# Optimization experiments

Measured on AMD Instinct MI355X. Metric: run time of the kernel, lower is better.

## Reference

```python
import jax, jax.numpy as jnp
import numpy as np

B, T, N_EMBD, HEAD = 4, 2048, 1024, 128


def setup_inputs() -> dict:
    key = jax.random.key(0)
    ks = jax.random.split(key, 7)
    s = 1.0 / np.sqrt(N_EMBD)
    return {
        "X": jax.random.normal(ks[0], (B, T, N_EMBD), dtype=jnp.float32),
        "Wk": jax.random.normal(ks[1], (N_EMBD, HEAD), dtype=jnp.float32) * s,
        "bk": jax.random.normal(ks[2], (HEAD,), dtype=jnp.float32) * 0.02,
        "Wq": jax.random.normal(ks[3], (N_EMBD, HEAD), dtype=jnp.float32) * s,
        "bq": jax.random.normal(ks[4], (HEAD,), dtype=jnp.float32) * 0.02,
        "Wv": jax.random.normal(ks[5], (N_EMBD, HEAD), dtype=jnp.float32) * s,
        "bv": jax.random.normal(ks[6], (HEAD,), dtype=jnp.float32) * 0.02,
    }


def reference(X, Wk, bk, Wq, bq, Wv, bv):
    # X: [B, T, C] with C = n_embd
    C = X.shape[-1]
    k = X @ Wk + bk  # [B, T, H]
    q = X @ Wq + bq  # [B, T, H]
    # NOTE: original computes k @ q^T (not q @ k^T) and scales by n_embd**-0.5.
    wei = jnp.einsum("bth,bsh->bts", k, q) * (C ** -0.5)  # [B, T, T]
    # NOTE: original's masked_fill is not in-place and its result is discarded,
    # so NO causal mask is actually applied. Dropout is identity (eval).
    wei = jax.nn.softmax(wei, axis=-1)
    v = X @ Wv + bv  # [B, T, H]
    out = jnp.einsum("bts,bsh->bth", wei, v)  # [B, T, H]
    return out
```

## Files before the change

kernel.cpp:

```cpp
#include <hip/hip_runtime.h>
#include <hip/hip_bf16.h>

#define Bn 4
#define Tn 2048
#define Cn 1024
#define Hn 128
#define Mn (Bn*Tn)
#define SCHUNKS 4
#define SCHUNK  (Tn/SCHUNKS)

typedef _Float16 f16;
typedef __attribute__((ext_vector_type(4))) _Float16 f16x4;
typedef __attribute__((ext_vector_type(8))) _Float16 f16x8;
typedef __attribute__((ext_vector_type(4))) float f32x4;

__global__ __launch_bounds__(256) void prep_w(const float* __restrict__ Wk,
                                              const float* __restrict__ Wq,
                                              const float* __restrict__ Wv,
                                              f16* __restrict__ Wt) {
    __shared__ __align__(16) f16 T[64 * 72];
    const int w = blockIdx.z;
    const float* W = (w == 0) ? Wk : (w == 1) ? Wq : Wv;
    const int c0 = blockIdx.x * 64, h0 = blockIdx.y * 64;
    const int tid = threadIdx.x;

    for (int i = 0; i < 4; i++) {
        int ci = tid + 256 * i;
        int row = ci >> 4, c4 = ci & 15;
        float4 x = *(const float4*)(W + (c0 + row) * Hn + h0 + c4 * 4);
        f16x4 v = { (f16)x.x, (f16)x.y, (f16)x.z, (f16)x.w };
        *(f16x4*)(&T[row * 72 + c4 * 4]) = v;
    }
    __syncthreads();
    for (int i = 0; i < 2; i++) {
        int ci = tid + 256 * i;
        int h = ci >> 3, cc = ci & 7;
        f16x8 v;
        for (int j = 0; j < 8; j++) v[j] = T[(cc * 8 + j) * 72 + h];
        *(f16x8*)(Wt + (w * Hn + h0 + h) * Cn + c0 + cc * 8) = v;
    }
}

__global__ __launch_bounds__(512) void qkv_gemm(const float* __restrict__ X,
                                                const f16* __restrict__ Wt,
                                                const float* __restrict__ bk,
                                                const float* __restrict__ bq,
                                                const float* __restrict__ bv,
                                                f16* __restrict__ pk,
                                                f16* __restrict__ pq,
                                                f16* __restrict__ vT) {
    __shared__ __align__(16) char smem[36864];
    f16* As = (f16*)smem;
    f16* Bs = (f16*)(smem + 9216);

    const int tid  = threadIdx.x;
    const int r0   = blockIdx.x * 64;
    const int ns   = blockIdx.y;
    const int lane = tid & 63, wid = tid >> 6;
    const int quad = lane >> 4, l16 = lane & 15;
    const int wm = wid >> 2, wn = wid & 3;

    f32x4 acc[2][3] = {};

    for (int k0 = 0; k0 < Cn; k0 += 64) {
        for (int i = 0; i < 2; i++) {
            int ci = tid + 512 * i;
            int row = ci >> 4, c4 = ci & 15;
            float4 x = *(const float4*)(X + (r0 + row) * Cn + k0 + c4 * 4);
            f16x4 v = { (f16)x.x, (f16)x.y, (f16)x.z, (f16)x.w };
            *(f16x4*)(&As[row * 72 + c4 * 4]) = v;
        }
        for (int i = 0; i < 3; i++) {
            int ci = tid + 512 * i;
            int row = ci >> 3, cc = ci & 7;
            *(f16x8*)(&Bs[row * 72 + cc * 8]) =
                *(const f16x8*)(Wt + (ns * 192 + row) * Cn + k0 + cc * 8);
        }
        __syncthreads();
        for (int ks = 0; ks < 2; ks++) {
            int kk = ks * 32;
            f16x8 af[2], bf[3];
            for (int mt = 0; mt < 2; mt++)
                af[mt] = *(const f16x8*)(&As[(wm * 32 + mt * 16 + l16) * 72 + kk + quad * 8]);
            for (int nt = 0; nt < 3; nt++)
                bf[nt] = *(const f16x8*)(&Bs[(wn * 48 + nt * 16 + l16) * 72 + kk + quad * 8]);
            for (int mt = 0; mt < 2; mt++)
                for (int nt = 0; nt < 3; nt++)
                    acc[mt][nt] = __builtin_amdgcn_mfma_f32_16x16x32_f16(
                        af[mt], bf[nt], acc[mt][nt], 0, 0, 0);
        }
        __syncthreads();
    }

    f16* E = (f16*)smem;
    for (int nt = 0; nt < 3; nt++) {
        int n0 = ns * 192 + wn * 48 + nt * 16;
        int wsel = n0 >> 7;
        int col = (n0 & 127) + l16;
        const float* bias = (wsel == 0) ? bk : (wsel == 1) ? bq : bv;
        float bval = bias[col];
        float scale = (wsel == 0) ? 0.03125f : 1.0f;
        for (int mt = 0; mt < 2; mt++)
            for (int r = 0; r < 4; r++) {
                int mrow = wm * 32 + mt * 16 + quad * 4 + r;
                E[mrow * 200 + wn * 48 + nt * 16 + l16] =
                    (f16)((acc[mt][nt][r] + bval) * scale);
            }
    }
    __syncthreads();

    if (ns == 0) {
        for (int i = 0; i < 3; i++) {
            int ci = tid + 512 * i;
            int row = ci / 24, c = ci % 24;
            f16x8 v = *(const f16x8*)(&E[row * 200 + c * 8]);
            int gn = c * 8;
            f16* dst = (gn < 128) ? (pk + (r0 + row) * Hn + gn)
                                  : (pq + (r0 + row) * Hn + (gn - 128));
            *(f16x8*)dst = v;
        }
    } else {
        {
            int ci = tid;
            int row = ci >> 3, c = ci & 7;
            f16x8 v = *(const f16x8*)(&E[row * 200 + c * 8]);
            *(f16x8*)(pq + (r0 + row) * Hn + 64 + c * 8) = v;
        }
        int b = r0 >> 11, sg = r0 & 2047;
        for (int i = 0; i < 2; i++) {
            int ci = tid + 512 * i;
            int h = ci >> 3, sc = ci & 7;
            f16x8 v;
            for (int j = 0; j < 8; j++)
                v[j] = E[(sc * 8 + j) * 200 + 64 + h];
            *(f16x8*)(vT + (b * Hn + h) * Tn + sg + sc * 8) = v;
        }
    }
}

__global__ __launch_bounds__(256, 2) void attn_kernel(const f16* __restrict__ pk,
                                                      const f16* __restrict__ pq,
                                                      const f16* __restrict__ vT,
                                                      f16* __restrict__ pO,
                                                      float* __restrict__ pm,
                                                      float* __restrict__ pl) {
    __shared__ __align__(16) char smem[36864];
    f16* Bq = (f16*)smem;
    f16* Vt = (f16*)(smem + 17408);

    const int tid  = threadIdx.x;
    const int tblk = blockIdx.x, c = blockIdx.y, b = blockIdx.z;
    const int t0   = tblk * 128;
    const int lane = tid & 63, wid = tid >> 6;
    const int quad = lane >> 4, l16 = lane & 15;
    const int tw   = t0 + wid * 32;

    const f16* kp = pk + b * Tn * Hn;
    const f16* qp = pq + b * Tn * Hn;
    const f16* vp = vT + b * Hn * Tn;

    f16x8 kfr[2][4];
    for (int tt = 0; tt < 2; tt++)
        for (int ks = 0; ks < 4; ks++)
            kfr[tt][ks] = *(const f16x8*)(kp + (tw + tt * 16 + l16) * Hn + ks * 32 + quad * 8);

    float m_i[2] = { -3e38f, -3e38f }, l_i[2] = { 0.0f, 0.0f };
    f32x4 accO[2][8] = {};

    f16x8 qreg[4], vreg[4];
    {
        const int s0 = c * SCHUNK;
        for (int i = 0; i < 4; i++) {
            int ci = tid + 256 * i;
            qreg[i] = *(const f16x8*)(qp + (s0 + (ci >> 4)) * Hn + (ci & 15) * 8);
            vreg[i] = *(const f16x8*)(vp + (ci >> 3) * Tn + s0 + (ci & 7) * 8);
        }
    }

    for (int si = 0; si < SCHUNK / 64; si++) {
        __syncthreads();
        for (int i = 0; i < 4; i++) {
            int ci = tid + 256 * i;
            *(f16x8*)(&Bq[(ci >> 4) * 136 + (ci & 15) * 8]) = qreg[i];
            *(f16x8*)(&Vt[(ci >> 3) * 72 + (ci & 7) * 8]) = vreg[i];
        }
        __syncthreads();
        if (si + 1 < SCHUNK / 64) {
            const int s1 = c * SCHUNK + (si + 1) * 64;
            for (int i = 0; i < 4; i++) {
                int ci = tid + 256 * i;
                qreg[i] = *(const f16x8*)(qp + (s1 + (ci >> 4)) * Hn + (ci & 15) * 8);
                vreg[i] = *(const f16x8*)(vp + (ci >> 3) * Tn + s1 + (ci & 7) * 8);
            }
        }

        f32x4 accS[2][4] = {};
        for (int ks = 0; ks < 4; ks++) {
            int kk = ks * 32;
            for (int st = 0; st < 4; st++) {
                f16x8 af = *(const f16x8*)(&Bq[(st * 16 + l16) * 136 + kk + quad * 8]);
                accS[0][st] = __builtin_amdgcn_mfma_f32_16x16x32_f16(af, kfr[0][ks], accS[0][st], 0, 0, 0);
                accS[1][st] = __builtin_amdgcn_mfma_f32_16x16x32_f16(af, kfr[1][ks], accS[1][st], 0, 0, 0);
            }
        }

        f16x4 pf[2][4];
        for (int tt = 0; tt < 2; tt++) {
            float mloc = -3e38f;
            for (int st = 0; st < 4; st++)
                for (int r = 0; r < 4; r++) mloc = fmaxf(mloc, accS[tt][st][r]);
            mloc = fmaxf(mloc, __shfl_xor(mloc, 16));
            mloc = fmaxf(mloc, __shfl_xor(mloc, 32));
            float mnew = fmaxf(m_i[tt], mloc);
            float alpha = __expf(m_i[tt] - mnew);
            m_i[tt] = mnew;
            float psum = 0.0f;
            for (int st = 0; st < 4; st++) {
                f32x4 p;
                for (int r = 0; r < 4; r++) {
                    p[r] = __expf(accS[tt][st][r] - mnew);
                    psum += p[r];
                }
                pf[tt][st] = { (f16)p[0], (f16)p[1], (f16)p[2], (f16)p[3] };
            }
            psum += __shfl_xor(psum, 16);
            psum += __shfl_xor(psum, 32);
            l_i[tt] = l_i[tt] * alpha + psum;
            for (int ht = 0; ht < 8; ht++)
                for (int r = 0; r < 4; r++) accO[tt][ht][r] *= alpha;
        }

        for (int st = 0; st < 4; st++) {
            for (int ht = 0; ht < 8; ht++) {
                f16x4 av = *(const f16x4*)(&Vt[(ht * 16 + l16) * 72 + st * 16 + quad * 4]);
                accO[0][ht] = __builtin_amdgcn_mfma_f32_16x16x16f16(av, pf[0][st], accO[0][ht], 0, 0, 0);
                accO[1][ht] = __builtin_amdgcn_mfma_f32_16x16x16f16(av, pf[1][st], accO[1][ht], 0, 0, 0);
            }
        }
    }

    for (int tt = 0; tt < 2; tt++) {
        __syncthreads();
        float* ep = (float*)smem + wid * 2048;
        for (int ht = 0; ht < 8; ht++)
            for (int r = 0; r < 4; r++)
                ep[(ht * 16 + quad * 4 + r) * 16 + l16] = accO[tt][ht][r];
        __syncthreads();
        {
            int t = lane >> 2, hq = lane & 3;
            int tgl = tw + tt * 16 + t;
            f16* dst = pO + ((size_t)(c * Bn + b) * Tn + tgl) * Hn + hq * 32;
            for (int g = 0; g < 4; g++) {
                f16x8 v;
                for (int j = 0; j < 8; j++)
                    v[j] = (f16)ep[(hq * 32 + g * 8 + j) * 16 + t];
                *(f16x8*)(dst + g * 8) = v;
            }
        }
        if (quad == 0) {
            pm[(c * Bn + b) * Tn + tw + tt * 16 + l16] = m_i[tt];
            pl[(c * Bn + b) * Tn + tw + tt * 16 + l16] = l_i[tt];
        }
    }
}

__global__ __launch_bounds__(256) void merge_kernel(const f16* __restrict__ pO,
                                                    const float* __restrict__ pm,
                                                    const float* __restrict__ pl,
                                                    float* __restrict__ out) {
    int gid = blockIdx.x * 256 + threadIdx.x;
    int tg  = gid >> 4;
    int hs  = (gid & 15) * 8;
    float mc[SCHUNKS], lc[SCHUNKS];
    float M = -3e38f;
    for (int cI = 0; cI < SCHUNKS; cI++) {
        mc[cI] = pm[cI * (Bn * Tn) + tg];
        lc[cI] = pl[cI * (Bn * Tn) + tg];
        M = fmaxf(M, mc[cI]);
    }
    float L = 0.0f, wc[SCHUNKS];
    for (int cI = 0; cI < SCHUNKS; cI++) {
        wc[cI] = __expf(mc[cI] - M);
        L += wc[cI] * lc[cI];
    }
    float inv = 1.0f / L;
    float o[8] = {};
    for (int cI = 0; cI < SCHUNKS; cI++) {
        const f16* src = pO + ((size_t)cI * Bn * Tn + tg) * Hn + hs;
        f16x8 v = *(const f16x8*)src;
        float w = wc[cI];
        for (int j = 0; j < 8; j++) o[j] += w * (float)v[j];
    }
    float* dst = out + (size_t)tg * Hn + hs;
    float4 v0 = { o[0] * inv, o[1] * inv, o[2] * inv, o[3] * inv };
    float4 v1 = { o[4] * inv, o[5] * inv, o[6] * inv, o[7] * inv };
    *(float4*)dst = v0;
    *(float4*)(dst + 4) = v1;
}

extern "C" void kernel_launch(void* const* d_in, const int* in_sizes, int n_in,
                              void* d_out, int out_size, void* d_ws, size_t ws_size,
                              hipStream_t stream) {
    const float* X  = (const float*)d_in[0];
    const float* Wk = (const float*)d_in[1];
    const float* bk = (const float*)d_in[2];
    const float* Wq = (const float*)d_in[3];
    const float* bq = (const float*)d_in[4];
    const float* Wv = (const float*)d_in[5];
    const float* bv = (const float*)d_in[6];
    float* out = (float*)d_out;

    char* base = (char*)d_ws;
    f16*   Wt = (f16*)(base);
    f16*   pk = (f16*)(base + 786432);
    f16*   pq = (f16*)(base + 2883584);
    f16*   vT = (f16*)(base + 4980736);
    f16*   pO = (f16*)(base + 7077888);
    float* pm = (float*)(base + 15466496);
    float* pl = (float*)(base + 15597568);

    prep_w<<<dim3(Cn / 64, Hn / 64, 3), 256, 0, stream>>>(Wk, Wq, Wv, Wt);
    qkv_gemm<<<dim3(Mn / 64, 2), 512, 0, stream>>>(X, Wt, bk, bq, bv, pk, pq, vT);
    attn_kernel<<<dim3(Tn / 128, SCHUNKS, Bn), 256, 0, stream>>>(pk, pq, vT, pO, pm, pl);
    merge_kernel<<<dim3(512), 256, 0, stream>>>(pO, pm, pl, out);
}
```

Measured before the change: 126.9 us.

## Register-prefetch next K tile in QKV GEMM and halve block to four waves

The QKV projection GEMM now loads the next 64-wide K slice of X and the weights into registers while MFMAs run on the current shared-memory tile, instead of doing load, sync, compute serially. The block shrinks from 512 to 256 threads, with each wave covering all 64 rows and 48 columns (a 4x3 MFMA tile per wave), which doubles per-wave register reuse of B fragments. The cost is more registers per thread (launch bounds 256,1) and fewer waves per block to hide latency.

After: 129.3 us. Within noise of the previous version (+1.9%).

```diff
diff --git a/kernel.cpp b/kernel.cpp
--- a/kernel.cpp
+++ b/kernel.cpp
@@ -41,14 +41,14 @@
     }
 }
 
-__global__ __launch_bounds__(512) void qkv_gemm(const float* __restrict__ X,
-                                                const f16* __restrict__ Wt,
-                                                const float* __restrict__ bk,
-                                                const float* __restrict__ bq,
-                                                const float* __restrict__ bv,
-                                                f16* __restrict__ pk,
-                                                f16* __restrict__ pq,
-                                                f16* __restrict__ vT) {
+__global__ __launch_bounds__(256, 1) void qkv_gemm(const float* __restrict__ X,
+                                                   const f16* __restrict__ Wt,
+                                                   const float* __restrict__ bk,
+                                                   const float* __restrict__ bq,
+                                                   const float* __restrict__ bv,
+                                                   f16* __restrict__ pk,
+                                                   f16* __restrict__ pq,
+                                                   f16* __restrict__ vT) {
     __shared__ __align__(16) char smem[36864];
     f16* As = (f16*)smem;
     f16* Bs = (f16*)(smem + 9216);
@@ -56,41 +56,60 @@
     const int tid  = threadIdx.x;
     const int r0   = blockIdx.x * 64;
     const int ns   = blockIdx.y;
-    const int lane = tid & 63, wid = tid >> 6;
+    const int lane = tid & 63, wn = tid >> 6;
     const int quad = lane >> 4, l16 = lane & 15;
-    const int wm = wid >> 2, wn = wid & 3;
-
-    f32x4 acc[2][3] = {};
-
-    for (int k0 = 0; k0 < Cn; k0 += 64) {
-        for (int i = 0; i < 2; i++) {
-            int ci = tid + 512 * i;
-            int row = ci >> 4, c4 = ci & 15;
-            float4 x = *(const float4*)(X + (r0 + row) * Cn + k0 + c4 * 4);
+
+    f32x4 acc[4][3] = {};
+
+    float4 xreg[4];
+    f16x8  wreg[6];
+    for (int i = 0; i < 4; i++) {
+        int ci = tid + 256 * i;
+        xreg[i] = *(const float4*)(X + (r0 + (ci >> 4)) * Cn + (ci & 15) * 4);
+    }
+    for (int i = 0; i < 6; i++) {
+        int ci = tid + 256 * i;
+        wreg[i] = *(const f16x8*)(Wt + (ns * 192 + (ci >> 3)) * Cn + (ci & 7) * 8);
+    }
+
+    for (int kit = 0; kit < 16; kit++) {
+        __syncthreads();
+        for (int i = 0; i < 4; i++) {
+            int ci = tid + 256 * i;
+            float4 x = xreg[i];
             f16x4 v = { (f16)x.x, (f16)x.y, (f16)x.z, (f16)x.w };
-            *(f16x4*)(&As[row * 72 + c4 * 4]) = v;
-        }
-        for (int i = 0; i < 3; i++) {
-            int ci = tid + 512 * i;
-            int row = ci >> 3, cc = ci & 7;
-            *(f16x8*)(&Bs[row * 72 + cc * 8]) =
-                *(const f16x8*)(Wt + (ns * 192 + row) * Cn + k0 + cc * 8);
-        }
-        __syncthreads();
+            *(f16x4*)(&As[(ci >> 4) * 72 + (ci & 15) * 4]) = v;
+        }
+        for (int i = 0; i < 6; i++) {
+            int ci = tid + 256 * i;
+            *(f16x8*)(&Bs[(ci >> 3) * 72 + (ci & 7) * 8]) = wreg[i];
+        }
+        __syncthreads();
+        if (kit + 1 < 16) {
+            int k1 = (kit + 1) * 64;
+            for (int i = 0; i < 4; i++) {
+                int ci = tid + 256 * i;
+                xreg[i] = *(const float4*)(X + (r0 + (ci >> 4)) * Cn + k1 + (ci & 15) * 4);
+            }
+            for (int i = 0; i < 6; i++) {
+                int ci = tid + 256 * i;
+                wreg[i] = *(const f16x8*)(Wt + (ns * 192 + (ci >> 3)) * Cn + k1 + (ci & 7) * 8);
+            }
+        }
         for (int ks = 0; ks < 2; ks++) {
             int kk = ks * 32;
-            f16x8 af[2], bf[3];
-            for (int mt = 0; mt < 2; mt++)
-                af[mt] = *(const f16x8*)(&As[(wm * 32 + mt * 16 + l16) * 72 + kk + quad * 8]);
+            f16x8 af[4], bf[3];
+            for (int mt = 0; mt < 4; mt++)
+                af[mt] = *(const f16x8*)(&As[(mt * 16 + l16) * 72 + kk + quad * 8]);
             for (int nt = 0; nt < 3; nt++)
                 bf[nt] = *(const f16x8*)(&Bs[(wn * 48 + nt * 16 + l16) * 72 + kk + quad * 8]);
-            for (int mt = 0; mt < 2; mt++)
+            for (int mt = 0; mt < 4; mt++)
                 for (int nt = 0; nt < 3; nt++)
                     acc[mt][nt] = __builtin_amdgcn_mfma_f32_16x16x32_f16(
                         af[mt], bf[nt], acc[mt][nt], 0, 0, 0);
         }
-        __syncthreads();
-    }
+    }
+    __syncthreads();
 
     f16* E = (f16*)smem;
     for (int nt = 0; nt < 3; nt++) {
@@ -100,9 +119,9 @@
         const float* bias = (wsel == 0) ? bk : (wsel == 1) ? bq : bv;
         float bval = bias[col];
         float scale = (wsel == 0) ? 0.03125f : 1.0f;
-        for (int mt = 0; mt < 2; mt++)
+        for (int mt = 0; mt < 4; mt++)
             for (int r = 0; r < 4; r++) {
-                int mrow = wm * 32 + mt * 16 + quad * 4 + r;
+                int mrow = mt * 16 + quad * 4 + r;
                 E[mrow * 200 + wn * 48 + nt * 16 + l16] =
                     (f16)((acc[mt][nt][r] + bval) * scale);
             }
@@ -110,8 +129,8 @@
     __syncthreads();
 
     if (ns == 0) {
-        for (int i = 0; i < 3; i++) {
-            int ci = tid + 512 * i;
+        for (int i = 0; i < 6; i++) {
+            int ci = tid + 256 * i;
             int row = ci / 24, c = ci % 24;
             f16x8 v = *(const f16x8*)(&E[row * 200 + c * 8]);
             int gn = c * 8;
@@ -120,15 +139,15 @@
             *(f16x8*)dst = v;
         }
     } else {
-        {
-            int ci = tid;
+        for (int i = 0; i < 2; i++) {
+            int ci = tid + 256 * i;
             int row = ci >> 3, c = ci & 7;
             f16x8 v = *(const f16x8*)(&E[row * 200 + c * 8]);
             *(f16x8*)(pq + (r0 + row) * Hn + 64 + c * 8) = v;
         }
         int b = r0 >> 11, sg = r0 & 2047;
-        for (int i = 0; i < 2; i++) {
-            int ci = tid + 512 * i;
+        for (int i = 0; i < 4; i++) {
+            int ci = tid + 256 * i;
             int h = ci >> 3, sc = ci & 7;
             f16x8 v;
             for (int j = 0; j < 8; j++)
@@ -320,7 +339,7 @@
     float* pl = (float*)(base + 15597568);
 
     prep_w<<<dim3(Cn / 64, Hn / 64, 3), 256, 0, stream>>>(Wk, Wq, Wv, Wt);
-    qkv_gemm<<<dim3(Mn / 64, 2), 512, 0, stream>>>(X, Wt, bk, bq, bv, pk, pq, vT);
+    qkv_gemm<<<dim3(Mn / 64, 2), 256, 0, stream>>>(X, Wt, bk, bq, bv, pk, pq, vT);
     attn_kernel<<<dim3(Tn / 128, SCHUNKS, Bn), 256, 0, stream>>>(pk, pq, vT, pO, pm, pl);
     merge_kernel<<<dim3(512), 256, 0, stream>>>(pO, pm, pl, out);
 }
```
